# Performance work log

Hardware: AMD Instinct MI355X
Metric: run time of the kernel (lower is better)

The kernel has to match this reference:

```python
import jax, jax.numpy as jnp
import numpy as np

T, N, F_IN, H, E = 48, 50000, 11, 256, 800000


def _gconv_gru(X, Hprev, Wx, bx, Wh, bh):
    # GConvGRU with ChebConv K=1: each conv is a plain linear (edge_index unused).
    # Wx: [3, H, in], Wh: [3, H, H]; gate order: z, r, h_tilde
    xg = jnp.einsum('ni,goi->gno', X, Wx) + bx[:, None, :]  # [3, N, H]
    z = jax.nn.sigmoid(xg[0] + Hprev @ Wh[0].T + bh[0])
    r = jax.nn.sigmoid(xg[1] + Hprev @ Wh[1].T + bh[1])
    h_til = jnp.tanh(xg[2] + (r * Hprev) @ Wh[2].T + bh[2])
    return z * Hprev + (1.0 - z) * h_til


def setup_inputs() -> dict:
    key = jax.random.key(0)
    ks = jax.random.split(key, 24)
    s = 0.05
    d = {
        'X_seq': jax.random.normal(ks[0], (T, N, F_IN), jnp.float32),
        'edge': jax.random.randint(ks[1], (2, E), 0, N, jnp.int64),
        # backbone GConvGRU (in=11 -> 256)
        'bb_Wx': jax.random.normal(ks[2], (3, H, F_IN), jnp.float32) * s,
        'bb_bx': jnp.zeros((3, H), jnp.float32),
        'bb_Wh': jax.random.normal(ks[3], (3, H, H), jnp.float32) * s,
        'bb_bh': jnp.zeros((3, H), jnp.float32),
        # gru_u (256 -> 256)
        'u_Wx': jax.random.normal(ks[4], (3, H, H), jnp.float32) * s,
        'u_bx': jnp.zeros((3, H), jnp.float32),
        'u_Wh': jax.random.normal(ks[5], (3, H, H), jnp.float32) * s,
        'u_bh': jnp.zeros((3, H), jnp.float32),
        # gru_sp (256 -> 256)
        'sp_Wx': jax.random.normal(ks[6], (3, H, H), jnp.float32) * s,
        'sp_bx': jnp.zeros((3, H), jnp.float32),
        'sp_Wh': jax.random.normal(ks[7], (3, H, H), jnp.float32) * s,
        'sp_bh': jnp.zeros((3, H), jnp.float32),
        # heads
        'Wu': jax.random.normal(ks[8], (3, H), jnp.float32) * s,
        'bu': jnp.zeros((3,), jnp.float32),
        'Ws': jax.random.normal(ks[9], (1, H), jnp.float32) * s,
        'bs': jnp.zeros((1,), jnp.float32),
        'Wp': jax.random.normal(ks[10], (1, H), jnp.float32) * s,
        'bp': jnp.zeros((1,), jnp.float32),
    }
    return d


def reference(X_seq, edge, bb_Wx, bb_bx, bb_Wh, bb_bh,
              u_Wx, u_bx, u_Wh, u_bh, sp_Wx, sp_bx, sp_Wh, sp_bh,
              Wu, bu, Ws, bs, Wp, bp):
    n = X_seq.shape[1]
    h = bb_Wh.shape[-1]
    H0 = jnp.zeros((n, h), X_seq.dtype)
    Hzero = jnp.zeros((n, h), X_seq.dtype)  # gru_u / gru_sp are called with H=None each step

    def step(Hprev, x):
        Hn = _gconv_gru(x, Hprev, bb_Wx, bb_bx, bb_Wh, bb_bh)
        hu = _gconv_gru(Hn, Hzero, u_Wx, u_bx, u_Wh, u_bh)
        hp = _gconv_gru(Hn, Hzero, sp_Wx, sp_bx, sp_Wh, sp_bh)
        u = hu @ Wu.T + bu                      # [N, 3]
        s = (hp @ Ws.T + bs)[:, 0]              # [N]
        p = (hp @ Wp.T + bp)[:, 0]              # [N]
        return Hn, (u, s, p)

    _, (U, S, P) = jax.lax.scan(step, H0, X_seq)
    return U, S, P
```

## Files before the change

kernel.cpp:

```cpp
#include <hip/hip_runtime.h>
#include <hip/hip_bf16.h>

#define NN 50000
#define TT 48
#define FIN 11
#define MB ((NN + 63) / 64)

typedef __bf16 bf16_t;
typedef __bf16 v8bf __attribute__((ext_vector_type(8)));
typedef __bf16 v2bf __attribute__((ext_vector_type(2)));
typedef float v4f __attribute__((ext_vector_type(4)));

__device__ __forceinline__ float sigm_(float x) {
  return __builtin_amdgcn_rcpf(1.0f + __expf(-x));
}
__device__ __forceinline__ float tanh_(float x) {
  return 1.0f - 2.0f * __builtin_amdgcn_rcpf(1.0f + __expf(2.0f * x));
}

#define MFMA16(A, B, C) C = __builtin_amdgcn_mfma_f32_16x16x32_bf16(A, B, C, 0, 0, 0)

__global__ void pack_w(const float* __restrict__ bbWx, const float* __restrict__ bbWh,
                       const float* __restrict__ uWx, const float* __restrict__ spWx,
                       bf16_t* __restrict__ PZ, bf16_t* __restrict__ PH,
                       bf16_t* __restrict__ PU) {
  int i0 = blockIdx.x * blockDim.x + threadIdx.x;
  int stride = gridDim.x * blockDim.x;
  for (int idx = i0; idx < 147456; idx += stride) {
    int e = idx & 7, lane = (idx >> 3) & 63, ch = idx >> 9;
    int w = ch / 36, r36 = ch - w * 36, kt = r36 >> 2, nf = (r36 >> 1) & 1, zr = r36 & 1;
    int l15 = lane & 15, q = lane >> 4;
    int c = w * 32 + nf * 16 + l15;
    int k = kt * 32 + q * 8 + e;
    float v = 0.f;
    if (k < 256) v = bbWh[(zr * 256 + c) * 256 + k];
    else if (k < 256 + FIN) v = bbWx[(zr * 256 + c) * FIN + (k - 256)];
    PZ[idx] = (bf16_t)v;
  }
  for (int idx = i0; idx < 73728; idx += stride) {
    int e = idx & 7, lane = (idx >> 3) & 63, ch = idx >> 9;
    int w = ch / 18, r18 = ch - w * 18, kt = r18 >> 1, nf = r18 & 1;
    int l15 = lane & 15, q = lane >> 4;
    int c = w * 32 + nf * 16 + l15;
    int k = kt * 32 + q * 8 + e;
    float v = 0.f;
    if (k < 256) v = bbWh[(512 + c) * 256 + k];
    else if (k < 256 + FIN) v = bbWx[(512 + c) * FIN + (k - 256)];
    PH[idx] = (bf16_t)v;
  }
  for (int idx = i0; idx < 262144; idx += stride) {
    int e = idx & 7, lane = (idx >> 3) & 63, ch = idx >> 9;
    int half = ch >> 8, r256 = ch & 255;
    int w = r256 >> 5, r32 = r256 & 31, kt = r32 >> 2, g = (r32 >> 1) & 1, nf = r32 & 1;
    int l15 = lane & 15, q = lane >> 4;
    int j = w * 32 + nf * 16 + l15;
    int gate = g * 2;
    int k = kt * 32 + q * 8 + e;
    const float* W = half ? spWx : uWx;
    PU[idx] = (bf16_t)W[(gate * 256 + j) * 256 + k];
  }
}

__global__ __launch_bounds__(512, 4) void fused_seq(
    const float* __restrict__ X,
    const bf16_t* __restrict__ PZ, const bf16_t* __restrict__ PH,
    const bf16_t* __restrict__ PU,
    const float* __restrict__ bbx, const float* __restrict__ bbh,
    const float* __restrict__ ubx, const float* __restrict__ ubh,
    const float* __restrict__ spbx, const float* __restrict__ spbh,
    const float* __restrict__ Wu, const float* __restrict__ buv,
    const float* __restrict__ Ws, const float* __restrict__ bsv,
    const float* __restrict__ Wp, const float* __restrict__ bpv,
    float* __restrict__ out) {
  __shared__ __align__(16) bf16_t Hm[64 * 256];
  __shared__ __align__(16) bf16_t Ha[64 * 32];
  __shared__ __align__(16) bf16_t Rm[64 * 256];
  char* const Hmb = (char*)Hm;
  char* const Hab = (char*)Ha;
  char* const Rmb = (char*)Rm;

  const int tid = threadIdx.x;
  const int lane = tid & 63, l15 = tid & 15, quad = (tid & 63) >> 4, wave = tid >> 6;
  const int rowBase = blockIdx.x * 64;
  const int srow = tid >> 3, sj = tid & 7, sm = rowBase + srow;

  const bf16_t* const pz0 = PZ + wave * 18432 + lane * 8;
  const bf16_t* const ph0 = PH + wave * 9216 + lane * 8;
  const bf16_t* const pu0 = PU + wave * 16384 + lane * 8;
  const bf16_t* const pu1 = PU + 131072 + wave * 16384 + lane * 8;

  {
    uint4 z4 = make_uint4(0u, 0u, 0u, 0u);
    for (int i = tid; i < 2048; i += 512) ((uint4*)Hmb)[i] = z4;
    if (tid < 256) ((uint4*)Hab)[tid] = z4;
  }
  __syncthreads();
  if (sm < NN) {
    bf16_t* xr = (bf16_t*)(Hab + (srow << 6));
    const float* xp = X + (long)sm * FIN;
    xr[sj] = (bf16_t)xp[sj];
    if (sj + 8 < FIN) xr[sj + 8] = (bf16_t)xp[sj + 8];
  }
  __syncthreads();

#pragma unroll 1
  for (int t = 0; t < TT; ++t) {
    v2bf zpk[4][2][2];

    {
      v4f az[4][2] = {};
#pragma unroll
      for (int kt = 0; kt < 9; ++kt) {
        v8bf a[4];
#pragma unroll
        for (int mf = 0; mf < 4; ++mf) {
          if (kt < 8)
            a[mf] = *(const v8bf*)(Hmb + ((mf * 16 + l15) << 9) +
                                   ((kt * 64 + quad * 16) ^ ((l15 & 7) << 4)));
          else
            a[mf] = *(const v8bf*)(Hab + ((mf * 16 + l15) << 6) + quad * 16);
        }
        const bf16_t* p = pz0 + kt * 2048;
        v8bf bz[2];
#pragma unroll
        for (int nf = 0; nf < 2; ++nf) bz[nf] = *(const v8bf*)(p + nf * 1024);
#pragma unroll
        for (int mf = 0; mf < 4; ++mf)
#pragma unroll
          for (int nf = 0; nf < 2; ++nf) MFMA16(a[mf], bz[nf], az[mf][nf]);
      }
#pragma unroll
      for (int nf = 0; nf < 2; ++nf) {
        const int c = wave * 32 + nf * 16 + l15;
        const float bz_ = bbx[c] + bbh[c];
#pragma unroll
        for (int mf = 0; mf < 4; ++mf)
#pragma unroll
          for (int rg = 0; rg < 4; ++rg)
            zpk[mf][nf][rg >> 1][rg & 1] = (bf16_t)sigm_(az[mf][nf][rg] + bz_);
      }
    }

    {
      v4f ar[4][2] = {};
#pragma unroll
      for (int kt = 0; kt < 9; ++kt) {
        v8bf a[4];
#pragma unroll
        for (int mf = 0; mf < 4; ++mf) {
          if (kt < 8)
            a[mf] = *(const v8bf*)(Hmb + ((mf * 16 + l15) << 9) +
                                   ((kt * 64 + quad * 16) ^ ((l15 & 7) << 4)));
          else
            a[mf] = *(const v8bf*)(Hab + ((mf * 16 + l15) << 6) + quad * 16);
        }
        const bf16_t* p = pz0 + kt * 2048 + 512;
        v8bf br[2];
#pragma unroll
        for (int nf = 0; nf < 2; ++nf) br[nf] = *(const v8bf*)(p + nf * 1024);
#pragma unroll
        for (int mf = 0; mf < 4; ++mf)
#pragma unroll
          for (int nf = 0; nf < 2; ++nf) MFMA16(a[mf], br[nf], ar[mf][nf]);
      }
#pragma unroll
      for (int nf = 0; nf < 2; ++nf) {
        const int c = wave * 32 + nf * 16 + l15;
        const float br_ = bbx[256 + c] + bbh[256 + c];
#pragma unroll
        for (int mf = 0; mf < 4; ++mf)
#pragma unroll
          for (int rg = 0; rg < 4; ++rg) {
            const int m = mf * 16 + quad * 4 + rg;
            const int off = (m << 9) + ((c * 2) ^ ((m & 7) << 4));
            const float hp = (float)*(const bf16_t*)(Hmb + off);
            *(bf16_t*)(Rmb + off) = (bf16_t)(sigm_(ar[mf][nf][rg] + br_) * hp);
          }
      }
    }
    __syncthreads();

    float xv0 = 0.f, xv1 = 0.f;
    if (t + 1 < TT && sm < NN) {
      const float* xp = X + ((long)(t + 1) * NN + sm) * FIN;
      xv0 = xp[sj];
      if (sj + 8 < FIN) xv1 = xp[sj + 8];
    }

    {
      v4f ah[4][2] = {};
#pragma unroll
      for (int kt = 0; kt < 9; ++kt) {
        v8bf a[4];
#pragma unroll
        for (int mf = 0; mf < 4; ++mf) {
          if (kt < 8)
            a[mf] = *(const v8bf*)(Rmb + ((mf * 16 + l15) << 9) +
                                   ((kt * 64 + quad * 16) ^ ((l15 & 7) << 4)));
          else
            a[mf] = *(const v8bf*)(Hab + ((mf * 16 + l15) << 6) + quad * 16);
        }
        const bf16_t* p = ph0 + kt * 1024;
        v8bf bh[2];
#pragma unroll
        for (int nf = 0; nf < 2; ++nf) bh[nf] = *(const v8bf*)(p + nf * 512);
#pragma unroll
        for (int mf = 0; mf < 4; ++mf)
#pragma unroll
          for (int nf = 0; nf < 2; ++nf) MFMA16(a[mf], bh[nf], ah[mf][nf]);
      }
#pragma unroll
      for (int nf = 0; nf < 2; ++nf) {
        const int c = wave * 32 + nf * 16 + l15;
        const float bh_ = bbx[512 + c] + bbh[512 + c];
#pragma unroll
        for (int mf = 0; mf < 4; ++mf)
#pragma unroll
          for (int rg = 0; rg < 4; ++rg) {
            const int m = mf * 16 + quad * 4 + rg;
            const int off = (m << 9) + ((c * 2) ^ ((m & 7) << 4));
            const float htl = tanh_(ah[mf][nf][rg] + bh_);
            const float z = (float)zpk[mf][nf][rg >> 1][rg & 1];
            const float hp = (float)*(const bf16_t*)(Hmb + off);
            *(bf16_t*)(Hmb + off) = (bf16_t)(z * hp + (1.f - z) * htl);
          }
      }
    }
    __syncthreads();

    {
      bf16_t* xr = (bf16_t*)(Hab + (srow << 6));
      xr[sj] = (bf16_t)xv0;
      if (sj + 8 < FIN) xr[sj + 8] = (bf16_t)xv1;
    }

#pragma unroll 1
    for (int half = 0; half < 2; ++half) {
      const bf16_t* puh = half ? pu1 : pu0;
      const float* gbx = half ? spbx : ubx;
      const float* gbh = half ? spbh : ubh;
      {
        v4f au[4][2] = {};
#pragma unroll
        for (int kt = 0; kt < 8; ++kt) {
          v8bf a[4];
#pragma unroll
          for (int mf = 0; mf < 4; ++mf)
            a[mf] = *(const v8bf*)(Hmb + ((mf * 16 + l15) << 9) +
                                   ((kt * 64 + quad * 16) ^ ((l15 & 7) << 4)));
          const bf16_t* p = puh + kt * 2048;
          v8bf bu[2];
#pragma unroll
          for (int nf = 0; nf < 2; ++nf) bu[nf] = *(const v8bf*)(p + nf * 512);
#pragma unroll
          for (int mf = 0; mf < 4; ++mf)
#pragma unroll
            for (int nf = 0; nf < 2; ++nf) MFMA16(a[mf], bu[nf], au[mf][nf]);
        }
#pragma unroll
        for (int nf = 0; nf < 2; ++nf) {
          const int j = wave * 32 + nf * 16 + l15;
          const float b0 = gbx[j] + gbh[j];
#pragma unroll
          for (int mf = 0; mf < 4; ++mf)
#pragma unroll
            for (int rg = 0; rg < 4; ++rg) {
              const int r = mf * 16 + quad * 4 + rg;
              *(bf16_t*)(Rmb + (r << 9) + ((j * 2) ^ ((r & 7) << 4))) =
                  (bf16_t)sigm_(au[mf][nf][rg] + b0);
            }
        }
      }
      {
        v4f au[4][2] = {};
#pragma unroll
        for (int kt = 0; kt < 8; ++kt) {
          v8bf a[4];
#pragma unroll
          for (int mf = 0; mf < 4; ++mf)
            a[mf] = *(const v8bf*)(Hmb + ((mf * 16 + l15) << 9) +
                                   ((kt * 64 + quad * 16) ^ ((l15 & 7) << 4)));
          const bf16_t* p = puh + kt * 2048 + 1024;
          v8bf bu[2];
#pragma unroll
          for (int nf = 0; nf < 2; ++nf) bu[nf] = *(const v8bf*)(p + nf * 512);
#pragma unroll
          for (int mf = 0; mf < 4; ++mf)
#pragma unroll
            for (int nf = 0; nf < 2; ++nf) MFMA16(a[mf], bu[nf], au[mf][nf]);
        }
#pragma unroll
        for (int nf = 0; nf < 2; ++nf) {
          const int j = wave * 32 + nf * 16 + l15;
          const float b1 = gbx[512 + j] + gbh[512 + j];
#pragma unroll
          for (int mf = 0; mf < 4; ++mf)
#pragma unroll
            for (int rg = 0; rg < 4; ++rg) {
              const int r = mf * 16 + quad * 4 + rg;
              bf16_t* cell = (bf16_t*)(Rmb + (r << 9) + ((j * 2) ^ ((r & 7) << 4)));
              const float zz = (float)*cell;
              const float ht = tanh_(au[mf][nf][rg] + b1);
              *cell = (bf16_t)((1.f - zz) * ht);
            }
        }
      }
      __syncthreads();
      if (half == 0) {
        if (tid < 192) {
          const int r = tid / 3, k = tid - r * 3, m = rowBase + r;
          if (m < NN) {
            float s = 0.f;
            for (int j = 0; j < 256; j += 8) {
              v8bf hv = *(const v8bf*)(Rmb + (r << 9) + ((j * 2) ^ ((r & 7) << 4)));
              const float* w = Wu + k * 256 + j;
#pragma unroll
              for (int jj = 0; jj < 8; ++jj) s += (float)hv[jj] * w[jj];
            }
            out[(long)t * (NN * 3) + (long)m * 3 + k] = s + buv[k];
          }
        }
      } else {
        if (tid < 128) {
          const int r = tid >> 1, which = tid & 1, m = rowBase + r;
          if (m < NN) {
            const float* W = which ? Wp : Ws;
            float s = 0.f;
            for (int j = 0; j < 256; j += 8) {
              v8bf hv = *(const v8bf*)(Rmb + (r << 9) + ((j * 2) ^ ((r & 7) << 4)));
#pragma unroll
              for (int jj = 0; jj < 8; ++jj) s += (float)hv[jj] * W[j + jj];
            }
            s += which ? bpv[0] : bsv[0];
            out[(long)TT * NN * 3 + (long)which * TT * NN + (long)t * NN + m] = s;
          }
        }
      }
      __syncthreads();
    }
  }
}

extern "C" void kernel_launch(void* const* d_in, const int* in_sizes, int n_in,
                              void* d_out, int out_size, void* d_ws, size_t ws_size,
                              hipStream_t stream) {
  const float* X    = (const float*)d_in[0];
  const float* bbWx = (const float*)d_in[2];
  const float* bbbx = (const float*)d_in[3];
  const float* bbWh = (const float*)d_in[4];
  const float* bbbh = (const float*)d_in[5];
  const float* uWx  = (const float*)d_in[6];
  const float* ubx  = (const float*)d_in[7];
  const float* ubh  = (const float*)d_in[9];
  const float* spWx = (const float*)d_in[10];
  const float* spbx = (const float*)d_in[11];
  const float* spbh = (const float*)d_in[13];
  const float* Wu   = (const float*)d_in[14];
  const float* buv  = (const float*)d_in[15];
  const float* Ws   = (const float*)d_in[16];
  const float* bsv  = (const float*)d_in[17];
  const float* Wp   = (const float*)d_in[18];
  const float* bpv  = (const float*)d_in[19];
  float* out = (float*)d_out;

  char* ws = (char*)d_ws;
  bf16_t* PZ = (bf16_t*)(ws);
  bf16_t* PH = (bf16_t*)(ws + 294912);
  bf16_t* PU = (bf16_t*)(ws + 442368);
  if (ws_size < (size_t)966656) return;

  pack_w<<<dim3(192), dim3(256), 0, stream>>>(bbWx, bbWh, uWx, spWx, PZ, PH, PU);
  fused_seq<<<dim3(MB), dim3(512), 0, stream>>>(X, PZ, PH, PU, bbbx, bbbh,
                                                ubx, ubh, spbx, spbh,
                                                Wu, buv, Ws, bsv, Wp, bpv, out);
}
```

Measured before the change: 10.70 ms.

## Process 128 rows per block with 16 waves, keep gate in registers

Doubles the rows per workgroup to 128 with 1024 threads. Two groups of 8 waves each handle 64 rows and share the same weight slices, so each block fetches its weights for twice as many rows. The z gate of the u/sp GRUs now stays in registers instead of going through an LDS write and read. Loads of X and stores to the output become nontemporal. LDS use per block roughly doubles and register pressure rises under launch_bounds(1024,4), which may lower occupancy or force spills.

```diff
diff --git a/kernel.cpp b/kernel.cpp
--- a/kernel.cpp
+++ b/kernel.cpp
@@ -4,7 +4,7 @@
 #define NN 50000
 #define TT 48
 #define FIN 11
-#define MB ((NN + 63) / 64)
+#define MB2 ((NN + 127) / 128)
 
 typedef __bf16 bf16_t;
 typedef __bf16 v8bf __attribute__((ext_vector_type(8)));
@@ -61,7 +61,7 @@
   }
 }
 
-__global__ __launch_bounds__(512, 4) void fused_seq(
+__global__ __launch_bounds__(1024, 4) void fused_seq(
     const float* __restrict__ X,
     const bf16_t* __restrict__ PZ, const bf16_t* __restrict__ PH,
     const bf16_t* __restrict__ PU,
@@ -72,27 +72,29 @@
     const float* __restrict__ Ws, const float* __restrict__ bsv,
     const float* __restrict__ Wp, const float* __restrict__ bpv,
     float* __restrict__ out) {
-  __shared__ __align__(16) bf16_t Hm[64 * 256];
-  __shared__ __align__(16) bf16_t Ha[64 * 32];
-  __shared__ __align__(16) bf16_t Rm[64 * 256];
+  __shared__ __align__(16) bf16_t Hm[128 * 256];
+  __shared__ __align__(16) bf16_t Ha[128 * 32];
+  __shared__ __align__(16) bf16_t Rm[128 * 256];
   char* const Hmb = (char*)Hm;
   char* const Hab = (char*)Ha;
   char* const Rmb = (char*)Rm;
 
   const int tid = threadIdx.x;
   const int lane = tid & 63, l15 = tid & 15, quad = (tid & 63) >> 4, wave = tid >> 6;
-  const int rowBase = blockIdx.x * 64;
+  const int wrow = (wave >> 3) * 64;
+  const int wv = wave & 7;
+  const int rowBase = blockIdx.x * 128;
   const int srow = tid >> 3, sj = tid & 7, sm = rowBase + srow;
 
-  const bf16_t* const pz0 = PZ + wave * 18432 + lane * 8;
-  const bf16_t* const ph0 = PH + wave * 9216 + lane * 8;
-  const bf16_t* const pu0 = PU + wave * 16384 + lane * 8;
-  const bf16_t* const pu1 = PU + 131072 + wave * 16384 + lane * 8;
+  const bf16_t* const pz0 = PZ + wv * 18432 + lane * 8;
+  const bf16_t* const ph0 = PH + wv * 9216 + lane * 8;
+  const bf16_t* const pu0 = PU + wv * 16384 + lane * 8;
+  const bf16_t* const pu1 = PU + 131072 + wv * 16384 + lane * 8;
 
   {
     uint4 z4 = make_uint4(0u, 0u, 0u, 0u);
-    for (int i = tid; i < 2048; i += 512) ((uint4*)Hmb)[i] = z4;
-    if (tid < 256) ((uint4*)Hab)[tid] = z4;
+    for (int i = tid; i < 4096; i += 1024) ((uint4*)Hmb)[i] = z4;
+    if (tid < 512) ((uint4*)Hab)[tid] = z4;
   }
   __syncthreads();
   if (sm < NN) {
@@ -114,11 +116,12 @@
         v8bf a[4];
 #pragma unroll
         for (int mf = 0; mf < 4; ++mf) {
+          const int row = wrow + mf * 16 + l15;
           if (kt < 8)
-            a[mf] = *(const v8bf*)(Hmb + ((mf * 16 + l15) << 9) +
+            a[mf] = *(const v8bf*)(Hmb + (row << 9) +
                                    ((kt * 64 + quad * 16) ^ ((l15 & 7) << 4)));
           else
-            a[mf] = *(const v8bf*)(Hab + ((mf * 16 + l15) << 6) + quad * 16);
+            a[mf] = *(const v8bf*)(Hab + (row << 6) + quad * 16);
         }
         const bf16_t* p = pz0 + kt * 2048;
         v8bf bz[2];
@@ -131,7 +134,7 @@
       }
 #pragma unroll
       for (int nf = 0; nf < 2; ++nf) {
-        const int c = wave * 32 + nf * 16 + l15;
+        const int c = wv * 32 + nf * 16 + l15;
         const float bz_ = bbx[c] + bbh[c];
 #pragma unroll
         for (int mf = 0; mf < 4; ++mf)
@@ -148,11 +151,12 @@
         v8bf a[4];
 #pragma unroll
         for (int mf = 0; mf < 4; ++mf) {
+          const int row = wrow + mf * 16 + l15;
           if (kt < 8)
-            a[mf] = *(const v8bf*)(Hmb + ((mf * 16 + l15) << 9) +
+            a[mf] = *(const v8bf*)(Hmb + (row << 9) +
                                    ((kt * 64 + quad * 16) ^ ((l15 & 7) << 4)));
           else
-            a[mf] = *(const v8bf*)(Hab + ((mf * 16 + l15) << 6) + quad * 16);
+            a[mf] = *(const v8bf*)(Hab + (row << 6) + quad * 16);
         }
         const bf16_t* p = pz0 + kt * 2048 + 512;
         v8bf br[2];
@@ -165,13 +169,13 @@
       }
 #pragma unroll
       for (int nf = 0; nf < 2; ++nf) {
-        const int c = wave * 32 + nf * 16 + l15;
+        const int c = wv * 32 + nf * 16 + l15;
         const float br_ = bbx[256 + c] + bbh[256 + c];
 #pragma unroll
         for (int mf = 0; mf < 4; ++mf)
 #pragma unroll
           for (int rg = 0; rg < 4; ++rg) {
-            const int m = mf * 16 + quad * 4 + rg;
+            const int m = wrow + mf * 16 + quad * 4 + rg;
             const int off = (m << 9) + ((c * 2) ^ ((m & 7) << 4));
             const float hp = (float)*(const bf16_t*)(Hmb + off);
             *(bf16_t*)(Rmb + off) = (bf16_t)(sigm_(ar[mf][nf][rg] + br_) * hp);
@@ -183,8 +187,8 @@
     float xv0 = 0.f, xv1 = 0.f;
     if (t + 1 < TT && sm < NN) {
       const float* xp = X + ((long)(t + 1) * NN + sm) * FIN;
-      xv0 = xp[sj];
-      if (sj + 8 < FIN) xv1 = xp[sj + 8];
+      xv0 = __builtin_nontemporal_load(xp + sj);
+      if (sj + 8 < FIN) xv1 = __builtin_nontemporal_load(xp + sj + 8);
     }
 
     {
@@ -194,11 +198,12 @@
         v8bf a[4];
 #pragma unroll
         for (int mf = 0; mf < 4; ++mf) {
+          const int row = wrow + mf * 16 + l15;
           if (kt < 8)
-            a[mf] = *(const v8bf*)(Rmb + ((mf * 16 + l15) << 9) +
+            a[mf] = *(const v8bf*)(Rmb + (row << 9) +
                                    ((kt * 64 + quad * 16) ^ ((l15 & 7) << 4)));
           else
-            a[mf] = *(const v8bf*)(Hab + ((mf * 16 + l15) << 6) + quad * 16);
+            a[mf] = *(const v8bf*)(Hab + (row << 6) + quad * 16);
         }
         const bf16_t* p = ph0 + kt * 1024;
         v8bf bh[2];
@@ -211,13 +216,13 @@
       }
 #pragma unroll
       for (int nf = 0; nf < 2; ++nf) {
-        const int c = wave * 32 + nf * 16 + l15;
+        const int c = wv * 32 + nf * 16 + l15;
         const float bh_ = bbx[512 + c] + bbh[512 + c];
 #pragma unroll
         for (int mf = 0; mf < 4; ++mf)
 #pragma unroll
           for (int rg = 0; rg < 4; ++rg) {
-            const int m = mf * 16 + quad * 4 + rg;
+            const int m = wrow + mf * 16 + quad * 4 + rg;
             const int off = (m << 9) + ((c * 2) ^ ((m & 7) << 4));
             const float htl = tanh_(ah[mf][nf][rg] + bh_);
             const float z = (float)zpk[mf][nf][rg >> 1][rg & 1];
@@ -239,15 +244,18 @@
       const bf16_t* puh = half ? pu1 : pu0;
       const float* gbx = half ? spbx : ubx;
       const float* gbh = half ? spbh : ubh;
+      v2bf zz2[4][2][2];
       {
         v4f au[4][2] = {};
 #pragma unroll
         for (int kt = 0; kt < 8; ++kt) {
           v8bf a[4];
 #pragma unroll
-          for (int mf = 0; mf < 4; ++mf)
-            a[mf] = *(const v8bf*)(Hmb + ((mf * 16 + l15) << 9) +
-                                   ((kt * 64 + quad * 16) ^ ((l15 & 7) << 4)));
+          for (int mf = 0; mf < 4; ++mf) {
+            const int row = wrow + mf * 16 + l15;
+            a[mf] = *(const v8bf*)(Hmb + (row << 9) +
+                                   ((kt * 64 + quad * 16) ^ ((l15 & 7) << 4)));
+          }
           const bf16_t* p = puh + kt * 2048;
           v8bf bu[2];
 #pragma unroll
@@ -259,16 +267,13 @@
         }
 #pragma unroll
         for (int nf = 0; nf < 2; ++nf) {
-          const int j = wave * 32 + nf * 16 + l15;
+          const int j = wv * 32 + nf * 16 + l15;
           const float b0 = gbx[j] + gbh[j];
 #pragma unroll
           for (int mf = 0; mf < 4; ++mf)
 #pragma unroll
-            for (int rg = 0; rg < 4; ++rg) {
-              const int r = mf * 16 + quad * 4 + rg;
-              *(bf16_t*)(Rmb + (r << 9) + ((j * 2) ^ ((r & 7) << 4))) =
-                  (bf16_t)sigm_(au[mf][nf][rg] + b0);
-            }
+            for (int rg = 0; rg < 4; ++rg)
+              zz2[mf][nf][rg >> 1][rg & 1] = (bf16_t)sigm_(au[mf][nf][rg] + b0);
         }
       }
       {
@@ -277,9 +282,11 @@
         for (int kt = 0; kt < 8; ++kt) {
           v8bf a[4];
 #pragma unroll
-          for (int mf = 0; mf < 4; ++mf)
-            a[mf] = *(const v8bf*)(Hmb + ((mf * 16 + l15) << 9) +
-                                   ((kt * 64 + quad * 16) ^ ((l15 & 7) << 4)));
+          for (int mf = 0; mf < 4; ++mf) {
+            const int row = wrow + mf * 16 + l15;
+            a[mf] = *(const v8bf*)(Hmb + (row << 9) +
+                                   ((kt * 64 + quad * 16) ^ ((l15 & 7) << 4)));
+          }
           const bf16_t* p = puh + kt * 2048 + 1024;
           v8bf bu[2];
 #pragma unroll
@@ -291,23 +298,23 @@
         }
 #pragma unroll
         for (int nf = 0; nf < 2; ++nf) {
-          const int j = wave * 32 + nf * 16 + l15;
+          const int j = wv * 32 + nf * 16 + l15;
           const float b1 = gbx[512 + j] + gbh[512 + j];
 #pragma unroll
           for (int mf = 0; mf < 4; ++mf)
 #pragma unroll
             for (int rg = 0; rg < 4; ++rg) {
-              const int r = mf * 16 + quad * 4 + rg;
-              bf16_t* cell = (bf16_t*)(Rmb + (r << 9) + ((j * 2) ^ ((r & 7) << 4)));
-              const float zz = (float)*cell;
+              const int r = wrow + mf * 16 + quad * 4 + rg;
+              const float zz = (float)zz2[mf][nf][rg >> 1][rg & 1];
               const float ht = tanh_(au[mf][nf][rg] + b1);
-              *cell = (bf16_t)((1.f - zz) * ht);
+              *(bf16_t*)(Rmb + (r << 9) + ((j * 2) ^ ((r & 7) << 4))) =
+                  (bf16_t)((1.f - zz) * ht);
             }
         }
       }
       __syncthreads();
       if (half == 0) {
-        if (tid < 192) {
+        if (tid < 384) {
           const int r = tid / 3, k = tid - r * 3, m = rowBase + r;
           if (m < NN) {
             float s = 0.f;
@@ -317,11 +324,12 @@
 #pragma unroll
               for (int jj = 0; jj < 8; ++jj) s += (float)hv[jj] * w[jj];
             }
-            out[(long)t * (NN * 3) + (long)m * 3 + k] = s + buv[k];
+            __builtin_nontemporal_store(s + buv[k],
+                                        &out[(long)t * (NN * 3) + (long)m * 3 + k]);
           }
         }
       } else {
-        if (tid < 128) {
+        if (tid < 256) {
           const int r = tid >> 1, which = tid & 1, m = rowBase + r;
           if (m < NN) {
             const float* W = which ? Wp : Ws;
@@ -332,7 +340,8 @@
               for (int jj = 0; jj < 8; ++jj) s += (float)hv[jj] * W[j + jj];
             }
             s += which ? bpv[0] : bsv[0];
-            out[(long)TT * NN * 3 + (long)which * TT * NN + (long)t * NN + m] = s;
+            __builtin_nontemporal_store(
+                s, &out[(long)TT * NN * 3 + (long)which * TT * NN + (long)t * NN + m]);
           }
         }
       }
@@ -370,7 +379,7 @@
   if (ws_size < (size_t)966656) return;
 
   pack_w<<<dim3(192), dim3(256), 0, stream>>>(bbWx, bbWh, uWx, spWx, PZ, PH, PU);
-  fused_seq<<<dim3(MB), dim3(512), 0, stream>>>(X, PZ, PH, PU, bbbx, bbbh,
-                                                ubx, ubh, spbx, spbh,
-                                                Wu, buv, Ws, bsv, Wp, bpv, out);
-}
+  fused_seq<<<dim3(MB2), dim3(1024), 0, stream>>>(X, PZ, PH, PU, bbbx, bbbh,
+                                                  ubx, ubh, spbx, spbh,
+                                                  Wu, buv, Ws, bsv, Wp, bpv, out);
+}
```

Result: slower. 11.73 ms (+9.6%).
